# Performance work log

Hardware: AMD Instinct MI355X
Metric: run time of the kernel (lower is better)

Reference implementation:

```python
import jax, jax.numpy as jnp
import numpy as np

N_NODES = 50000
N_EDGES = 300000
IN_FEATS = 128
N_HIDDEN = 64
N_HEADS = 4
N_CLASSES = 47
NEG_SLOPE = 0.2


def setup_inputs() -> dict:
    key = jax.random.key(0)
    ks = jax.random.split(key, 16)
    s = 0.1
    inp = {
        "x": jax.random.normal(ks[0], (N_NODES, IN_FEATS), jnp.float32),
        "src": jax.random.randint(ks[1], (N_EDGES,), 0, N_NODES, jnp.int64 if jax.config.jax_enable_x64 else jnp.int32),
        "dst": jax.random.randint(ks[2], (N_EDGES,), 0, N_NODES, jnp.int64 if jax.config.jax_enable_x64 else jnp.int32),
        # layer 1: in_feats -> (heads, hidden)
        "W1": jax.random.normal(ks[3], (IN_FEATS, N_HEADS * N_HIDDEN), jnp.float32) * s,
        "al1": jax.random.normal(ks[4], (N_HEADS, N_HIDDEN), jnp.float32) * s,
        "ar1": jax.random.normal(ks[5], (N_HEADS, N_HIDDEN), jnp.float32) * s,
        "b1": jnp.zeros((N_HEADS * N_HIDDEN,), jnp.float32),
        # layer 2: heads*hidden -> (heads, hidden)
        "W2": jax.random.normal(ks[6], (N_HEADS * N_HIDDEN, N_HEADS * N_HIDDEN), jnp.float32) * s,
        "al2": jax.random.normal(ks[7], (N_HEADS, N_HIDDEN), jnp.float32) * s,
        "ar2": jax.random.normal(ks[8], (N_HEADS, N_HIDDEN), jnp.float32) * s,
        "b2": jnp.zeros((N_HEADS * N_HIDDEN,), jnp.float32),
        # layer 3: heads*hidden -> (1, n_classes)
        "W3": jax.random.normal(ks[9], (N_HEADS * N_HIDDEN, N_CLASSES), jnp.float32) * s,
        "al3": jax.random.normal(ks[10], (1, N_CLASSES), jnp.float32) * s,
        "ar3": jax.random.normal(ks[11], (1, N_CLASSES), jnp.float32) * s,
        "b3": jnp.zeros((N_CLASSES,), jnp.float32),
    }
    return inp


def gat_conv(h, src, dst, W, al, ar, b, n_nodes):
    """DGL GATConv (shared src/dst projection, edge-softmax over dst)."""
    H, D = al.shape
    feat = (h @ W).reshape(n_nodes, H, D)              # [N,H,D]
    el = jnp.sum(feat * al[None], axis=-1)             # [N,H]
    er = jnp.sum(feat * ar[None], axis=-1)             # [N,H]
    e = jax.nn.leaky_relu(el[src] + er[dst], NEG_SLOPE)  # [E,H]
    emax = jax.ops.segment_max(e, dst, num_segments=n_nodes)  # [N,H]
    emax = jnp.where(jnp.isfinite(emax), emax, 0.0)    # empty segments
    ee = jnp.exp(e - emax[dst])                        # [E,H]
    denom = jax.ops.segment_sum(ee, dst, num_segments=n_nodes)  # [N,H]
    alpha = ee / jnp.maximum(denom[dst], 1e-9)         # [E,H]
    msg = feat[src] * alpha[..., None]                 # [E,H,D]
    out = jax.ops.segment_sum(msg, dst, num_segments=n_nodes)   # [N,H,D]
    return out + b.reshape(1, H, D)


def reference(x, src, dst, W1, al1, ar1, b1, W2, al2, ar2, b2, W3, al3, ar3, b3):
    n = x.shape[0]
    h = gat_conv(x, src, dst, W1, al1, ar1, b1, n).reshape(n, -1)  # flatten heads
    h = gat_conv(h, src, dst, W2, al2, ar2, b2, n).reshape(n, -1)
    h = gat_conv(h, src, dst, W3, al3, ar3, b3, n)                 # [N,1,C]
    return h.mean(axis=1)                                          # [N,C]
```

## Files before the change

kernel.cpp:

```cpp
#include <hip/hip_runtime.h>
#include <cstddef>

#define GAT_N 50000
#define GAT_E 300000
#define SCAN_B 256

typedef short bf16x8 __attribute__((ext_vector_type(8)));
typedef float f32x4  __attribute__((ext_vector_type(4)));

__device__ __forceinline__ ushort f2bf(float f) {
    unsigned u = __float_as_uint(f);
    return (ushort)((u + 0x7fffu + ((u >> 16) & 1u)) >> 16);
}
__device__ __forceinline__ float bf2f(ushort h) {
    return __uint_as_float((unsigned)h << 16);
}


__global__ __launch_bounds__(256) void zero_ints(int* __restrict__ a, int n) {
    int i = blockIdx.x * blockDim.x + threadIdx.x;
    int stride = gridDim.x * blockDim.x;
    for (; i < n; i += stride) a[i] = 0;
}

__global__ __launch_bounds__(256) void count_k(
    const int* __restrict__ dst, int* __restrict__ cnt, int E)
{
    int e = blockIdx.x * blockDim.x + threadIdx.x;
    if (e < E) atomicAdd(&cnt[dst[e]], 1);
}

__global__ __launch_bounds__(256) void csr_partial(
    const int* __restrict__ cnt, int* __restrict__ partials, int N, int chunk)
{
    __shared__ int red[256];
    int b = blockIdx.x, t = threadIdx.x;
    int s = 0;
    for (int i = t; i < chunk; i += 256) {
        int idx = b * chunk + i;
        if (idx < N) s += cnt[idx];
    }
    red[t] = s;
    __syncthreads();
    for (int off = 128; off > 0; off >>= 1) {
        if (t < off) red[t] += red[t + off];
        __syncthreads();
    }
    if (t == 0) partials[b] = red[0];
}

__global__ __launch_bounds__(SCAN_B) void csr_scanp(
    int* __restrict__ partials, int* __restrict__ rowptr, int N)
{
    __shared__ int sc[SCAN_B];
    int t = threadIdx.x;
    int v = partials[t];
    sc[t] = v;
    __syncthreads();
    for (int off = 1; off < SCAN_B; off <<= 1) {
        int u = (t >= off) ? sc[t - off] : 0;
        __syncthreads();
        sc[t] += u;
        __syncthreads();
    }
    partials[t] = sc[t] - v;
    if (t == SCAN_B - 1) rowptr[N] = sc[t];
}

__global__ __launch_bounds__(256) void csr_write(
    const int* __restrict__ cnt, const int* __restrict__ partials,
    int* __restrict__ rowptr, int N, int chunk)
{
    __shared__ int sc[256];
    int b = blockIdx.x, t = threadIdx.x;
    int idx = b * chunk + t;
    int v = (t < chunk && idx < N) ? cnt[idx] : 0;
    sc[t] = v;
    __syncthreads();
    for (int off = 1; off < 256; off <<= 1) {
        int u = (t >= off) ? sc[t - off] : 0;
        __syncthreads();
        sc[t] += u;
        __syncthreads();
    }
    if (t < chunk && idx < N) rowptr[idx] = partials[b] + sc[t] - v;
}

__global__ __launch_bounds__(256) void scatter_k(
    const int* __restrict__ src, const int* __restrict__ dst,
    const int* __restrict__ rowptr, int* __restrict__ cursor,
    int* __restrict__ ssrc, int* __restrict__ sdst, int E)
{
    int e = blockIdx.x * blockDim.x + threadIdx.x;
    if (e >= E) return;
    int d = dst[e];
    int p = rowptr[d] + atomicAdd(&cursor[d], 1);
    ssrc[p] = src[e];
    sdst[p] = d;
}


__global__ __launch_bounds__(256) void convert_x(
    const float* __restrict__ x, ushort* __restrict__ Xh, ushort* __restrict__ Xl,
    long total4)
{
    long i = (long)blockIdx.x * blockDim.x + threadIdx.x;
    long stride = (long)gridDim.x * blockDim.x;
    for (; i < total4; i += stride) {
        float4 v = *(const float4*)(x + i * 4);
        ushort4 h, lo;
        h.x = f2bf(v.x); lo.x = f2bf(v.x - bf2f(h.x));
        h.y = f2bf(v.y); lo.y = f2bf(v.y - bf2f(h.y));
        h.z = f2bf(v.z); lo.z = f2bf(v.z - bf2f(h.z));
        h.w = f2bf(v.w); lo.w = f2bf(v.w - bf2f(h.w));
        *(ushort4*)(Xh + i * 4) = h;
        *(ushort4*)(Xl + i * 4) = lo;
    }
}

__global__ __launch_bounds__(256) void convert_w(
    const float* __restrict__ W, ushort* __restrict__ Wth, ushort* __restrict__ Wtl,
    int K, int M, int Mp)
{
    int idx = blockIdx.x * blockDim.x + threadIdx.x;
    if (idx >= Mp * K) return;
    int c = idx / K, k = idx - c * K;
    float v = (c < M) ? W[(size_t)k * M + c] : 0.f;
    ushort h = f2bf(v);
    Wth[idx] = h;
    Wtl[idx] = f2bf(v - bf2f(h));
}


#define LDK 40

__global__ __launch_bounds__(256) void gemm_feat(
    const ushort* __restrict__ Ah, const ushort* __restrict__ Al,
    const ushort* __restrict__ Wh, const ushort* __restrict__ Wl,
    const float* __restrict__ alw, const float* __restrict__ arw,
    float* __restrict__ feat, float* __restrict__ el, float* __restrict__ er,
    int N, int K, int M, int H, int D, int ldF)
{
    __shared__ ushort As_h[64 * LDK];
    __shared__ ushort As_l[64 * LDK];
    __shared__ ushort Bs_h[128 * LDK];
    __shared__ ushort Bs_l[128 * LDK];

    const int m0 = blockIdx.x * 64;
    const int n0 = blockIdx.y * 128;
    const int t = threadIdx.x;
    const int w = t >> 6, lane = t & 63;
    const int lr = lane & 15, lg = lane >> 4;
    const int wr = (w >> 1) * 32, wc = (w & 1) * 64;

    f32x4 acc[2][4] = {};

    for (int k0 = 0; k0 < K; k0 += 32) {
        {
            int row = t >> 2, kk = (t & 3) * 8;
            bf16x8 vh = {}, vl = {};
            int gr = m0 + row;
            if (gr < N) {
                vh = *(const bf16x8*)(Ah + (size_t)gr * K + k0 + kk);
                vl = *(const bf16x8*)(Al + (size_t)gr * K + k0 + kk);
            }
            *(bf16x8*)&As_h[row * LDK + kk] = vh;
            *(bf16x8*)&As_l[row * LDK + kk] = vl;
        }
        #pragma unroll
        for (int l = 0; l < 2; ++l) {
            int idx = t + l * 256;
            int row = idx >> 2, kk = (idx & 3) * 8;
            *(bf16x8*)&Bs_h[row * LDK + kk] = *(const bf16x8*)(Wh + (size_t)(n0 + row) * K + k0 + kk);
            *(bf16x8*)&Bs_l[row * LDK + kk] = *(const bf16x8*)(Wl + (size_t)(n0 + row) * K + k0 + kk);
        }
        __syncthreads();

        bf16x8 a_h[2], a_l[2];
        #pragma unroll
        for (int fi = 0; fi < 2; ++fi) {
            a_h[fi] = *(const bf16x8*)&As_h[(wr + fi * 16 + lr) * LDK + lg * 8];
            a_l[fi] = *(const bf16x8*)&As_l[(wr + fi * 16 + lr) * LDK + lg * 8];
        }
        #pragma unroll
        for (int fj = 0; fj < 4; ++fj) {
            bf16x8 b_h = *(const bf16x8*)&Bs_h[(wc + fj * 16 + lr) * LDK + lg * 8];
            bf16x8 b_l = *(const bf16x8*)&Bs_l[(wc + fj * 16 + lr) * LDK + lg * 8];
            #pragma unroll
            for (int fi = 0; fi < 2; ++fi) {
                acc[fi][fj] = __builtin_amdgcn_mfma_f32_16x16x32_bf16(a_h[fi], b_h, acc[fi][fj], 0, 0, 0);
                acc[fi][fj] = __builtin_amdgcn_mfma_f32_16x16x32_bf16(a_l[fi], b_h, acc[fi][fj], 0, 0, 0);
                acc[fi][fj] = __builtin_amdgcn_mfma_f32_16x16x32_bf16(a_h[fi], b_l, acc[fi][fj], 0, 0, 0);
            }
        }
        __syncthreads();
    }

    #pragma unroll
    for (int fi = 0; fi < 2; ++fi) {
        #pragma unroll
        for (int q = 0; q < 4; ++q) {
            int row = m0 + wr + fi * 16 + 4 * lg + q;
            if (row < N) {
                #pragma unroll
                for (int fj = 0; fj < 4; ++fj) {
                    int col = n0 + wc + fj * 16 + lr;
                    if (col < M) feat[(size_t)row * ldF + col] = acc[fi][fj][q];
                }
            }
        }
    }

    const int head = (n0 + wc) / D;
    if (head < H) {
        float alv[4], arv[4];
        #pragma unroll
        for (int fj = 0; fj < 4; ++fj) {
            int col = n0 + wc + fj * 16 + lr;
            alv[fj] = (col < M) ? alw[col] : 0.f;
            arv[fj] = (col < M) ? arw[col] : 0.f;
        }
        #pragma unroll
        for (int fi = 0; fi < 2; ++fi) {
            #pragma unroll
            for (int q = 0; q < 4; ++q) {
                float s1 = 0.f, s2 = 0.f;
                #pragma unroll
                for (int fj = 0; fj < 4; ++fj) {
                    s1 = fmaf(acc[fi][fj][q], alv[fj], s1);
                    s2 = fmaf(acc[fi][fj][q], arv[fj], s2);
                }
                #pragma unroll
                for (int mask = 1; mask <= 8; mask <<= 1) {
                    s1 += __shfl_xor(s1, mask);
                    s2 += __shfl_xor(s2, mask);
                }
                int row = m0 + wr + fi * 16 + 4 * lg + q;
                if (lr == 0 && row < N) {
                    el[(size_t)row * H + head] = s1;
                    er[(size_t)row * H + head] = s2;
                }
            }
        }
    }
}


__global__ __launch_bounds__(256) void edge_score4(
    const int* __restrict__ ssrc, const int* __restrict__ sdst,
    const float* __restrict__ el, const float* __restrict__ er,
    float* __restrict__ sc, int E)
{
    int p = blockIdx.x * blockDim.x + threadIdx.x;
    if (p >= E) return;
    int s = ssrc[p], d = sdst[p];
    float4 a = *(const float4*)(el + (size_t)s * 4);
    float4 b = *(const float4*)(er + (size_t)d * 4);
    float4 v;
    v.x = a.x + b.x; v.x = v.x > 0.f ? v.x : 0.2f * v.x;
    v.y = a.y + b.y; v.y = v.y > 0.f ? v.y : 0.2f * v.y;
    v.z = a.z + b.z; v.z = v.z > 0.f ? v.z : 0.2f * v.z;
    v.w = a.w + b.w; v.w = v.w > 0.f ? v.w : 0.2f * v.w;
    *(float4*)(sc + (size_t)p * 4) = v;
}

__global__ __launch_bounds__(256) void edge_score1(
    const int* __restrict__ ssrc, const int* __restrict__ sdst,
    const float* __restrict__ el, const float* __restrict__ er,
    float* __restrict__ sc, int E)
{
    int p = blockIdx.x * blockDim.x + threadIdx.x;
    if (p >= E) return;
    float v = el[ssrc[p]] + er[sdst[p]];
    sc[p] = v > 0.f ? v : 0.2f * v;
}


__global__ __launch_bounds__(256) void node_aggr256(
    const int* __restrict__ rowptr, const int* __restrict__ ssrc,
    const float* __restrict__ sc, const float* __restrict__ feat,
    const float* __restrict__ bias,
    ushort* __restrict__ Ah_out, ushort* __restrict__ Al_out, int N)
{
    int n = blockIdx.x * 4 + (threadIdx.x >> 6);
    if (n >= N) return;
    int lane = threadIdx.x & 63;
    int h = lane >> 4, sub = lane & 15;
    int beg = rowptr[n], end = rowptr[n + 1];

    float m = -__builtin_inff();
    for (int j = beg + sub; j < end; j += 16)
        m = fmaxf(m, sc[(size_t)j * 4 + h]);
    #pragma unroll
    for (int mask = 1; mask <= 8; mask <<= 1)
        m = fmaxf(m, __shfl_xor(m, mask));

    float denom = 0.f;
    for (int j = beg + sub; j < end; j += 16)
        denom += __expf(sc[(size_t)j * 4 + h] - m);
    #pragma unroll
    for (int mask = 1; mask <= 8; mask <<= 1)
        denom += __shfl_xor(denom, mask);

    float inv = 1.f / fmaxf(denom, 1e-9f);
    float ax = 0.f, ay = 0.f, az = 0.f, aw = 0.f;
    int j = beg;
    for (; j + 4 <= end; j += 4) {
        int s0 = ssrc[j + 0], s1 = ssrc[j + 1], s2 = ssrc[j + 2], s3 = ssrc[j + 3];
        float w0 = __expf(sc[(size_t)(j + 0) * 4 + h] - m);
        float w1 = __expf(sc[(size_t)(j + 1) * 4 + h] - m);
        float w2 = __expf(sc[(size_t)(j + 2) * 4 + h] - m);
        float w3 = __expf(sc[(size_t)(j + 3) * 4 + h] - m);
        float4 f0 = *(const float4*)(feat + (size_t)s0 * 256 + lane * 4);
        float4 f1 = *(const float4*)(feat + (size_t)s1 * 256 + lane * 4);
        float4 f2 = *(const float4*)(feat + (size_t)s2 * 256 + lane * 4);
        float4 f3 = *(const float4*)(feat + (size_t)s3 * 256 + lane * 4);
        ax = fmaf(w0, f0.x, fmaf(w1, f1.x, fmaf(w2, f2.x, fmaf(w3, f3.x, ax))));
        ay = fmaf(w0, f0.y, fmaf(w1, f1.y, fmaf(w2, f2.y, fmaf(w3, f3.y, ay))));
        az = fmaf(w0, f0.z, fmaf(w1, f1.z, fmaf(w2, f2.z, fmaf(w3, f3.z, az))));
        aw = fmaf(w0, f0.w, fmaf(w1, f1.w, fmaf(w2, f2.w, fmaf(w3, f3.w, aw))));
    }
    for (; j < end; ++j) {
        float wgt = __expf(sc[(size_t)j * 4 + h] - m);
        int s = ssrc[j];
        float4 f = *(const float4*)(feat + (size_t)s * 256 + lane * 4);
        ax = fmaf(wgt, f.x, ax);
        ay = fmaf(wgt, f.y, ay);
        az = fmaf(wgt, f.z, az);
        aw = fmaf(wgt, f.w, aw);
    }
    float v0 = fmaf(ax, inv, bias[lane * 4 + 0]);
    float v1 = fmaf(ay, inv, bias[lane * 4 + 1]);
    float v2 = fmaf(az, inv, bias[lane * 4 + 2]);
    float v3 = fmaf(aw, inv, bias[lane * 4 + 3]);
    ushort4 hh, lo;
    hh.x = f2bf(v0); lo.x = f2bf(v0 - bf2f(hh.x));
    hh.y = f2bf(v1); lo.y = f2bf(v1 - bf2f(hh.y));
    hh.z = f2bf(v2); lo.z = f2bf(v2 - bf2f(hh.z));
    hh.w = f2bf(v3); lo.w = f2bf(v3 - bf2f(hh.w));
    *(ushort4*)(Ah_out + (size_t)n * 256 + lane * 4) = hh;
    *(ushort4*)(Al_out + (size_t)n * 256 + lane * 4) = lo;
}

__global__ __launch_bounds__(256) void node_aggr47(
    const int* __restrict__ rowptr, const int* __restrict__ ssrc,
    const float* __restrict__ sc, const float* __restrict__ feat,
    const float* __restrict__ bias, float* __restrict__ out, int N)
{
    int n = blockIdx.x * 4 + (threadIdx.x >> 6);
    if (n >= N) return;
    int lane = threadIdx.x & 63;
    int beg = rowptr[n], end = rowptr[n + 1];

    float m = -__builtin_inff();
    for (int j = beg + lane; j < end; j += 64)
        m = fmaxf(m, sc[j]);
    #pragma unroll
    for (int mask = 1; mask <= 32; mask <<= 1)
        m = fmaxf(m, __shfl_xor(m, mask));

    float denom = 0.f;
    for (int j = beg + lane; j < end; j += 64)
        denom += __expf(sc[j] - m);
    #pragma unroll
    for (int mask = 1; mask <= 32; mask <<= 1)
        denom += __shfl_xor(denom, mask);

    float inv = 1.f / fmaxf(denom, 1e-9f);
    float acc = 0.f;
    int j = beg;
    for (; j + 4 <= end; j += 4) {
        int s0 = ssrc[j + 0], s1 = ssrc[j + 1], s2 = ssrc[j + 2], s3 = ssrc[j + 3];
        float w0 = __expf(sc[j + 0] - m);
        float w1 = __expf(sc[j + 1] - m);
        float w2 = __expf(sc[j + 2] - m);
        float w3 = __expf(sc[j + 3] - m);
        float f0 = (lane < 47) ? feat[(size_t)s0 * 48 + lane] : 0.f;
        float f1 = (lane < 47) ? feat[(size_t)s1 * 48 + lane] : 0.f;
        float f2 = (lane < 47) ? feat[(size_t)s2 * 48 + lane] : 0.f;
        float f3 = (lane < 47) ? feat[(size_t)s3 * 48 + lane] : 0.f;
        acc = fmaf(w0, f0, fmaf(w1, f1, fmaf(w2, f2, fmaf(w3, f3, acc))));
    }
    for (; j < end; ++j) {
        float wgt = __expf(sc[j] - m);
        int s = ssrc[j];
        float f = (lane < 47) ? feat[(size_t)s * 48 + lane] : 0.f;
        acc = fmaf(wgt, f, acc);
    }
    if (lane < 47)
        out[(size_t)n * 47 + lane] = fmaf(acc, inv, bias[lane]);
}


extern "C" void kernel_launch(void* const* d_in, const int* in_sizes, int n_in,
                              void* d_out, int out_size, void* d_ws, size_t ws_size,
                              hipStream_t stream) {
    const float* x   = (const float*)d_in[0];
    const int*   src = (const int*)d_in[1];
    const int*   dst = (const int*)d_in[2];
    const float* W1  = (const float*)d_in[3];
    const float* al1 = (const float*)d_in[4];
    const float* ar1 = (const float*)d_in[5];
    const float* b1  = (const float*)d_in[6];
    const float* W2  = (const float*)d_in[7];
    const float* al2 = (const float*)d_in[8];
    const float* ar2 = (const float*)d_in[9];
    const float* b2  = (const float*)d_in[10];
    const float* W3  = (const float*)d_in[11];
    const float* al3 = (const float*)d_in[12];
    const float* ar3 = (const float*)d_in[13];
    const float* b3  = (const float*)d_in[14];
    float* out = (float*)d_out;

    const int N = GAT_N, E = GAT_E;
    const int chunk = (N + SCAN_B - 1) / SCAN_B;

    char* wsb = (char*)d_ws;
    size_t o = 0;
    float*  feat  = (float*)(wsb + o);  o += (size_t)N * 256 * 4;
    ushort* Ah    = (ushort*)(wsb + o); o += (size_t)N * 256 * 2;
    ushort* Al    = (ushort*)(wsb + o); o += (size_t)N * 256 * 2;
    float*  el    = (float*)(wsb + o);  o += (size_t)N * 4 * 4;
    float*  er    = (float*)(wsb + o);  o += (size_t)N * 4 * 4;
    int* rowptr   = (int*)(wsb + o);    o += (size_t)(N + 1) * 4;
    int* cnt      = (int*)(wsb + o);    o += (size_t)N * 4;
    int* cursor   = (int*)(wsb + o);    o += (size_t)N * 4;
    int* ssrc     = (int*)(wsb + o);    o += (size_t)E * 4;
    int* sdst     = (int*)(wsb + o);    o += (size_t)E * 4;
    float* scbuf  = (float*)(wsb + o);  o += (size_t)E * 4 * 4;
    int* partials = (int*)(wsb + o);    o += (size_t)SCAN_B * 4;
    ushort* Wt1h  = (ushort*)(wsb + o); o += (size_t)256 * 128 * 2;
    ushort* Wt1l  = (ushort*)(wsb + o); o += (size_t)256 * 128 * 2;
    ushort* Wt2h  = (ushort*)(wsb + o); o += (size_t)256 * 256 * 2;
    ushort* Wt2l  = (ushort*)(wsb + o); o += (size_t)256 * 256 * 2;
    ushort* Wt3h  = (ushort*)(wsb + o); o += (size_t)128 * 256 * 2;
    ushort* Wt3l  = (ushort*)(wsb + o); o += (size_t)128 * 256 * 2;
    ushort* Xh = Ah;
    ushort* Xl = Al;

    dim3 blk(256);
    int gE = (E + 255) / 256;
    int gN = (N + 3) / 4;
    dim3 gemmG((N + 63) / 64, 2);
    dim3 gemmG3((N + 63) / 64, 1);

    zero_ints<<<64, blk, 0, stream>>>(cnt, 2 * N);
    count_k<<<gE, blk, 0, stream>>>(dst, cnt, E);
    csr_partial<<<SCAN_B, blk, 0, stream>>>(cnt, partials, N, chunk);
    csr_scanp<<<1, SCAN_B, 0, stream>>>(partials, rowptr, N);
    csr_write<<<SCAN_B, blk, 0, stream>>>(cnt, partials, rowptr, N, chunk);
    scatter_k<<<gE, blk, 0, stream>>>(src, dst, rowptr, cursor, ssrc, sdst, E);

    convert_x<<<2048, blk, 0, stream>>>(x, Xh, Xl, (long)N * 128 / 4);
    convert_w<<<(256 * 128 + 255) / 256, blk, 0, stream>>>(W1, Wt1h, Wt1l, 128, 256, 256);
    convert_w<<<(256 * 256 + 255) / 256, blk, 0, stream>>>(W2, Wt2h, Wt2l, 256, 256, 256);
    convert_w<<<(128 * 256 + 255) / 256, blk, 0, stream>>>(W3, Wt3h, Wt3l, 256, 47, 128);

    gemm_feat<<<gemmG, blk, 0, stream>>>(Xh, Xl, Wt1h, Wt1l, al1, ar1,
                                         feat, el, er, N, 128, 256, 4, 64, 256);
    edge_score4<<<gE, blk, 0, stream>>>(ssrc, sdst, el, er, scbuf, E);
    node_aggr256<<<gN, blk, 0, stream>>>(rowptr, ssrc, scbuf, feat, b1, Ah, Al, N);

    gemm_feat<<<gemmG, blk, 0, stream>>>(Ah, Al, Wt2h, Wt2l, al2, ar2,
                                         feat, el, er, N, 256, 256, 4, 64, 256);
    edge_score4<<<gE, blk, 0, stream>>>(ssrc, sdst, el, er, scbuf, E);
    node_aggr256<<<gN, blk, 0, stream>>>(rowptr, ssrc, scbuf, feat, b2, Ah, Al, N);

    gemm_feat<<<gemmG3, blk, 0, stream>>>(Ah, Al, Wt3h, Wt3l, al3, ar3,
                                          feat, el, er, N, 256, 47, 1, 47, 48);
    edge_score1<<<gE, blk, 0, stream>>>(ssrc, sdst, el, er, scbuf, E);
    node_aggr47<<<gN, blk, 0, stream>>>(rowptr, ssrc, scbuf, feat, b3, out, N);
}
```

Before: 311.5 us.

## Double-buffer GEMM tiles with direct global-to-LDS loads

Rewrites the gemm_feat tile staging to use global_load_lds, which writes 16-byte chunks straight into shared memory in an MFMA-fragment-friendly layout. It adds a double buffer so the next K-tile loads while the current one is multiplied. This is meant to cut register round-trips and exposed global-load latency in the projection GEMM. It doubles LDS use, clamps out-of-range rows instead of zeroing them, and relies on the hardware's async LDS-load ordering being handled by the existing barriers.

```diff
diff --git a/kernel.cpp b/kernel.cpp
--- a/kernel.cpp
+++ b/kernel.cpp
@@ -7,6 +7,7 @@
 
 typedef short bf16x8 __attribute__((ext_vector_type(8)));
 typedef float f32x4  __attribute__((ext_vector_type(4)));
+typedef unsigned int u32;
 
 __device__ __forceinline__ ushort f2bf(float f) {
     unsigned u = __float_as_uint(f);
@@ -14,6 +15,12 @@
 }
 __device__ __forceinline__ float bf2f(ushort h) {
     return __uint_as_float((unsigned)h << 16);
+}
+
+__device__ __forceinline__ void gload16(const ushort* g, ushort* l) {
+    __builtin_amdgcn_global_load_lds(
+        (const __attribute__((address_space(1))) u32*)g,
+        (__attribute__((address_space(3))) u32*)l, 16, 0, 0);
 }
 
 
@@ -132,8 +139,6 @@
 }
 
 
-#define LDK 40
-
 __global__ __launch_bounds__(256) void gemm_feat(
     const ushort* __restrict__ Ah, const ushort* __restrict__ Al,
     const ushort* __restrict__ Wh, const ushort* __restrict__ Wl,
@@ -141,10 +146,7 @@
     float* __restrict__ feat, float* __restrict__ el, float* __restrict__ er,
     int N, int K, int M, int H, int D, int ldF)
 {
-    __shared__ ushort As_h[64 * LDK];
-    __shared__ ushort As_l[64 * LDK];
-    __shared__ ushort Bs_h[128 * LDK];
-    __shared__ ushort Bs_l[128 * LDK];
+    __shared__ ushort lds[2 * 12288];
 
     const int m0 = blockIdx.x * 64;
     const int n0 = blockIdx.y * 128;
@@ -152,40 +154,68 @@
     const int w = t >> 6, lane = t & 63;
     const int lr = lane & 15, lg = lane >> 4;
     const int wr = (w >> 1) * 32, wc = (w & 1) * 64;
+    const int NK = K >> 5;
+
+    const ushort* srcp[6];
+    u32 lbase[6];
+    #pragma unroll
+    for (int l = 0; l < 6; ++l) {
+        int ub = l * 256 + w * 64;
+        int u = ub + lane;
+        const ushort* s;
+        if (u < 512) {
+            int half = u >> 8;
+            int v = u & 255;
+            int rowblk = v >> 6, kc = (v >> 4) & 3, r = v & 15;
+            int grow = m0 + rowblk * 16 + r;
+            grow = grow < N ? grow : N - 1;
+            s = (half ? Al : Ah) + (size_t)grow * K + kc * 8;
+        } else {
+            int v = u - 512;
+            int half = v >> 9;
+            int b = v & 511;
+            int cb = b >> 6, kc = (b >> 4) & 3, c = b & 15;
+            int gcol = n0 + cb * 16 + c;
+            s = (half ? Wl : Wh) + (size_t)gcol * K + kc * 8;
+        }
+        srcp[l] = s;
+        lbase[l] = (u32)(ub * 8);
+    }
 
     f32x4 acc[2][4] = {};
 
-    for (int k0 = 0; k0 < K; k0 += 32) {
-        {
-            int row = t >> 2, kk = (t & 3) * 8;
-            bf16x8 vh = {}, vl = {};
-            int gr = m0 + row;
-            if (gr < N) {
-                vh = *(const bf16x8*)(Ah + (size_t)gr * K + k0 + kk);
-                vl = *(const bf16x8*)(Al + (size_t)gr * K + k0 + kk);
+    #pragma unroll
+    for (int l = 0; l < 6; ++l) {
+        gload16(srcp[l], &lds[lbase[l]]);
+        srcp[l] += 32;
+    }
+    __syncthreads();
+
+    int cur = 0;
+    for (int kt = 0; kt < NK; ++kt) {
+        if (kt + 1 < NK) {
+            int nb = (cur ^ 1) * 12288;
+            #pragma unroll
+            for (int l = 0; l < 6; ++l) {
+                gload16(srcp[l], &lds[nb + lbase[l]]);
+                srcp[l] += 32;
             }
-            *(bf16x8*)&As_h[row * LDK + kk] = vh;
-            *(bf16x8*)&As_l[row * LDK + kk] = vl;
-        }
-        #pragma unroll
-        for (int l = 0; l < 2; ++l) {
-            int idx = t + l * 256;
-            int row = idx >> 2, kk = (idx & 3) * 8;
-            *(bf16x8*)&Bs_h[row * LDK + kk] = *(const bf16x8*)(Wh + (size_t)(n0 + row) * K + k0 + kk);
-            *(bf16x8*)&Bs_l[row * LDK + kk] = *(const bf16x8*)(Wl + (size_t)(n0 + row) * K + k0 + kk);
-        }
-        __syncthreads();
-
+        }
+        const ushort* buf = lds + cur * 12288;
+        const int rb = (w >> 1) * 2;
+        const int cbb = (w & 1) * 4;
         bf16x8 a_h[2], a_l[2];
         #pragma unroll
         for (int fi = 0; fi < 2; ++fi) {
-            a_h[fi] = *(const bf16x8*)&As_h[(wr + fi * 16 + lr) * LDK + lg * 8];
-            a_l[fi] = *(const bf16x8*)&As_l[(wr + fi * 16 + lr) * LDK + lg * 8];
+            int idx = ((rb + fi) * 4 + lg) * 128 + lr * 8;
+            a_h[fi] = *(const bf16x8*)&buf[idx];
+            a_l[fi] = *(const bf16x8*)&buf[2048 + idx];
         }
         #pragma unroll
         for (int fj = 0; fj < 4; ++fj) {
-            bf16x8 b_h = *(const bf16x8*)&Bs_h[(wc + fj * 16 + lr) * LDK + lg * 8];
-            bf16x8 b_l = *(const bf16x8*)&Bs_l[(wc + fj * 16 + lr) * LDK + lg * 8];
+            int idx = ((cbb + fj) * 4 + lg) * 128 + lr * 8;
+            bf16x8 b_h = *(const bf16x8*)&buf[4096 + idx];
+            bf16x8 b_l = *(const bf16x8*)&buf[8192 + idx];
             #pragma unroll
             for (int fi = 0; fi < 2; ++fi) {
                 acc[fi][fj] = __builtin_amdgcn_mfma_f32_16x16x32_bf16(a_h[fi], b_h, acc[fi][fj], 0, 0, 0);
@@ -194,6 +224,7 @@
             }
         }
         __syncthreads();
+        cur ^= 1;
     }
 
     #pragma unroll
```

New measurement: 325.3 us. 1.04x slower.

## Double-buffer feature GEMM with direct global-to-LDS loads and 64x64 tiles

Applied to the files above, without the earlier changes.

Rewrites the split-bf16 feature GEMM to use 64x64 output tiles (one 16-row strip per wave) and doubles the y-grid to match. Operand tiles are moved straight from global memory into LDS with global_load_lds 16-byte transfers into a double-buffered layout, so the next K-slice loads while the current one feeds the MFMAs. This is meant to cut register staging and load latency in the GEMM. The cost is less A-tile reuse per block and more blocks. It also depends on the compiler waiting for the asynchronous LDS writes before each barrier.

```diff
diff --git a/kernel.cpp b/kernel.cpp
--- a/kernel.cpp
+++ b/kernel.cpp
@@ -7,6 +7,7 @@
 
 typedef short bf16x8 __attribute__((ext_vector_type(8)));
 typedef float f32x4  __attribute__((ext_vector_type(4)));
+typedef unsigned int u32;
 
 __device__ __forceinline__ ushort f2bf(float f) {
     unsigned u = __float_as_uint(f);
@@ -14,6 +15,12 @@
 }
 __device__ __forceinline__ float bf2f(ushort h) {
     return __uint_as_float((unsigned)h << 16);
+}
+
+__device__ __forceinline__ void gload16(const ushort* g, ushort* l) {
+    __builtin_amdgcn_global_load_lds(
+        (const __attribute__((address_space(1))) u32*)g,
+        (__attribute__((address_space(3))) u32*)l, 16, 0, 0);
 }
 
 
@@ -132,8 +139,6 @@
 }
 
 
-#define LDK 40
-
 __global__ __launch_bounds__(256) void gemm_feat(
     const ushort* __restrict__ Ah, const ushort* __restrict__ Al,
     const ushort* __restrict__ Wh, const ushort* __restrict__ Wl,
@@ -141,105 +146,106 @@
     float* __restrict__ feat, float* __restrict__ el, float* __restrict__ er,
     int N, int K, int M, int H, int D, int ldF)
 {
-    __shared__ ushort As_h[64 * LDK];
-    __shared__ ushort As_l[64 * LDK];
-    __shared__ ushort Bs_h[128 * LDK];
-    __shared__ ushort Bs_l[128 * LDK];
+    __shared__ ushort lds[2 * 8192];
 
     const int m0 = blockIdx.x * 64;
-    const int n0 = blockIdx.y * 128;
+    const int n0 = blockIdx.y * 64;
     const int t = threadIdx.x;
     const int w = t >> 6, lane = t & 63;
     const int lr = lane & 15, lg = lane >> 4;
-    const int wr = (w >> 1) * 32, wc = (w & 1) * 64;
-
-    f32x4 acc[2][4] = {};
-
-    for (int k0 = 0; k0 < K; k0 += 32) {
-        {
-            int row = t >> 2, kk = (t & 3) * 8;
-            bf16x8 vh = {}, vl = {};
-            int gr = m0 + row;
-            if (gr < N) {
-                vh = *(const bf16x8*)(Ah + (size_t)gr * K + k0 + kk);
-                vl = *(const bf16x8*)(Al + (size_t)gr * K + k0 + kk);
+    const int NK = K >> 5;
+
+    const ushort* srcp[4];
+    u32 lbase[4];
+    {
+        int v = w * 64 + lane;
+        int blk = v >> 6, kc = (v >> 4) & 3, rc = v & 15;
+        int grow = m0 + blk * 16 + rc;
+        grow = grow < N ? grow : N - 1;
+        int gcol = n0 + blk * 16 + rc;
+        srcp[0] = Ah + (size_t)grow * K + kc * 8;
+        srcp[1] = Al + (size_t)grow * K + kc * 8;
+        srcp[2] = Wh + (size_t)gcol * K + kc * 8;
+        srcp[3] = Wl + (size_t)gcol * K + kc * 8;
+        #pragma unroll
+        for (int l = 0; l < 4; ++l)
+            lbase[l] = (u32)((l * 256 + w * 64) * 8);
+    }
+
+    f32x4 acc[4] = {};
+
+    #pragma unroll
+    for (int l = 0; l < 4; ++l) {
+        gload16(srcp[l], &lds[lbase[l]]);
+        srcp[l] += 32;
+    }
+    __syncthreads();
+
+    int cur = 0;
+    for (int kt = 0; kt < NK; ++kt) {
+        if (kt + 1 < NK) {
+            int nb = (cur ^ 1) * 8192;
+            #pragma unroll
+            for (int l = 0; l < 4; ++l) {
+                gload16(srcp[l], &lds[nb + lbase[l]]);
+                srcp[l] += 32;
             }
-            *(bf16x8*)&As_h[row * LDK + kk] = vh;
-            *(bf16x8*)&As_l[row * LDK + kk] = vl;
         }
-        #pragma unroll
-        for (int l = 0; l < 2; ++l) {
-            int idx = t + l * 256;
-            int row = idx >> 2, kk = (idx & 3) * 8;
-            *(bf16x8*)&Bs_h[row * LDK + kk] = *(const bf16x8*)(Wh + (size_t)(n0 + row) * K + k0 + kk);
-            *(bf16x8*)&Bs_l[row * LDK + kk] = *(const bf16x8*)(Wl + (size_t)(n0 + row) * K + k0 + kk);
-        }
-        __syncthreads();
-
-        bf16x8 a_h[2], a_l[2];
-        #pragma unroll
-        for (int fi = 0; fi < 2; ++fi) {
-            a_h[fi] = *(const bf16x8*)&As_h[(wr + fi * 16 + lr) * LDK + lg * 8];
-            a_l[fi] = *(const bf16x8*)&As_l[(wr + fi * 16 + lr) * LDK + lg * 8];
-        }
+        const ushort* buf = lds + cur * 8192;
+        int aidx = (w * 4 + lg) * 128 + lr * 8;
+        bf16x8 a_h = *(const bf16x8*)&buf[aidx];
+        bf16x8 a_l = *(const bf16x8*)&buf[2048 + aidx];
         #pragma unroll
         for (int fj = 0; fj < 4; ++fj) {
-            bf16x8 b_h = *(const bf16x8*)&Bs_h[(wc + fj * 16 + lr) * LDK + lg * 8];
-            bf16x8 b_l = *(const bf16x8*)&Bs_l[(wc + fj * 16 + lr) * LDK + lg * 8];
+            int bidx = (fj * 4 + lg) * 128 + lr * 8;
+            bf16x8 b_h = *(const bf16x8*)&buf[4096 + bidx];
+            bf16x8 b_l = *(const bf16x8*)&buf[6144 + bidx];
+            acc[fj] = __builtin_amdgcn_mfma_f32_16x16x32_bf16(a_h, b_h, acc[fj], 0, 0, 0);
+            acc[fj] = __builtin_amdgcn_mfma_f32_16x16x32_bf16(a_l, b_h, acc[fj], 0, 0, 0);
+            acc[fj] = __builtin_amdgcn_mfma_f32_16x16x32_bf16(a_h, b_l, acc[fj], 0, 0, 0);
+        }
+        __syncthreads();
+        cur ^= 1;
+    }
+
+    #pragma unroll
+    for (int q = 0; q < 4; ++q) {
+        int row = m0 + w * 16 + 4 * lg + q;
+        if (row < N) {
             #pragma unroll
-            for (int fi = 0; fi < 2; ++fi) {
-                acc[fi][fj] = __builtin_amdgcn_mfma_f32_16x16x32_bf16(a_h[fi], b_h, acc[fi][fj], 0, 0, 0);
-                acc[fi][fj] = __builtin_amdgcn_mfma_f32_16x16x32_bf16(a_l[fi], b_h, acc[fi][fj], 0, 0, 0);
-                acc[fi][fj] = __builtin_amdgcn_mfma_f32_16x16x32_bf16(a_h[fi], b_l, acc[fi][fj], 0, 0, 0);
+            for (int fj = 0; fj < 4; ++fj) {
+                int col = n0 + fj * 16 + lr;
+                if (col < M) feat[(size_t)row * ldF + col] = acc[fj][q];
             }
         }
-        __syncthreads();
-    }
-
-    #pragma unroll
-    for (int fi = 0; fi < 2; ++fi) {
-        #pragma unroll
-        for (int q = 0; q < 4; ++q) {
-            int row = m0 + wr + fi * 16 + 4 * lg + q;
-            if (row < N) {
-                #pragma unroll
-                for (int fj = 0; fj < 4; ++fj) {
-                    int col = n0 + wc + fj * 16 + lr;
-                    if (col < M) feat[(size_t)row * ldF + col] = acc[fi][fj][q];
-                }
-            }
-        }
-    }
-
-    const int head = (n0 + wc) / D;
+    }
+
+    const int head = n0 / D;
     if (head < H) {
         float alv[4], arv[4];
         #pragma unroll
         for (int fj = 0; fj < 4; ++fj) {
-            int col = n0 + wc + fj * 16 + lr;
+            int col = n0 + fj * 16 + lr;
             alv[fj] = (col < M) ? alw[col] : 0.f;
             arv[fj] = (col < M) ? arw[col] : 0.f;
         }
         #pragma unroll
-        for (int fi = 0; fi < 2; ++fi) {
+        for (int q = 0; q < 4; ++q) {
+            float s1 = 0.f, s2 = 0.f;
             #pragma unroll
-            for (int q = 0; q < 4; ++q) {
-                float s1 = 0.f, s2 = 0.f;
-                #pragma unroll
-                for (int fj = 0; fj < 4; ++fj) {
-                    s1 = fmaf(acc[fi][fj][q], alv[fj], s1);
-                    s2 = fmaf(acc[fi][fj][q], arv[fj], s2);
-                }
-                #pragma unroll
-                for (int mask = 1; mask <= 8; mask <<= 1) {
-                    s1 += __shfl_xor(s1, mask);
-                    s2 += __shfl_xor(s2, mask);
-                }
-                int row = m0 + wr + fi * 16 + 4 * lg + q;
-                if (lr == 0 && row < N) {
-                    el[(size_t)row * H + head] = s1;
-                    er[(size_t)row * H + head] = s2;
-                }
+            for (int fj = 0; fj < 4; ++fj) {
+                s1 = fmaf(acc[fj][q], alv[fj], s1);
+                s2 = fmaf(acc[fj][q], arv[fj], s2);
+            }
+            #pragma unroll
+            for (int mask = 1; mask <= 8; mask <<= 1) {
+                s1 += __shfl_xor(s1, mask);
+                s2 += __shfl_xor(s2, mask);
+            }
+            int row = m0 + w * 16 + 4 * lg + q;
+            if (lr == 0 && row < N) {
+                el[(size_t)row * H + head] = s1;
+                er[(size_t)row * H + head] = s2;
             }
         }
     }
@@ -441,7 +447,7 @@
     dim3 blk(256);
     int gE = (E + 255) / 256;
     int gN = (N + 3) / 4;
-    dim3 gemmG((N + 63) / 64, 2);
+    dim3 gemmG((N + 63) / 64, 4);
     dim3 gemmG3((N + 63) / 64, 1);
 
     zero_ints<<<64, blk, 0, stream>>>(cnt, 2 * N);
```

After: 325.5 us. 4.5% more time.
